# Kernel tuning notes

Measured on AMD Instinct MI355X. Metric: run time of the kernel, lower is better.

## Reference

```python
import jax, jax.numpy as jnp
import numpy as np

NUM_BINS = 128  # 32 mid-band bins + 96 bottom-band bins
LN_EPS = 1e-5


def _mlp_scores(desc, W1, b1, g1, be1, W2, b2, Ws, bs):
    # Linear -> LayerNorm -> SiLU -> Linear -> score head
    h = desc @ W1 + b1
    mu = h.mean(-1, keepdims=True)
    var = h.var(-1, keepdims=True)
    h = (h - mu) * jax.lax.rsqrt(var + LN_EPS) * g1 + be1
    h = h * jax.nn.sigmoid(h)  # SiLU
    feat = h @ W2 + b2
    scores = (feat @ Ws + bs)[..., 0]  # [B, N]
    return scores


def _grid_ids(kpts, H, W):
    x = kpts[..., 0]
    y = kpts[..., 1]
    mid = (y > 0.2 * H) & (y <= 0.5 * H)
    btm = y > 0.5 * H
    mgx = jnp.clip((x / W * 8).astype(jnp.int32), 0, 7)
    mgy = jnp.clip(((y - 0.2 * H) / (0.3 * H) * 4).astype(jnp.int32), 0, 3)
    bgx = jnp.clip((x / W * 16).astype(jnp.int32), 0, 15)
    bgy = jnp.clip(((y - 0.5 * H) / (0.5 * H) * 6).astype(jnp.int32), 0, 5)
    gid = jnp.where(btm, 32 + bgy * 16 + bgx, jnp.where(mid, mgy * 8 + mgx, -1))
    return gid  # [B, N], -1 = not in any grid band


def _select_one(scores, gid, top_k):
    # strict-'>' loop in the original), then compact + top-k fallback.
    N = scores.shape[0]
    valid = gid >= 0
    seg = jnp.where(valid, gid, NUM_BINS)  # dump invalid pts in dummy bin
    binmax = jax.ops.segment_max(scores, seg, num_segments=NUM_BINS + 1)
    is_win = valid & (scores == binmax[seg])
    winner_idx = jax.ops.segment_min(
        jnp.where(is_win, jnp.arange(N), N), seg, num_segments=NUM_BINS + 1
    )[:NUM_BINS]  # N = empty bin sentinel
    bin_valid = winner_idx < N
    # stable sort: non-empty bins first, preserving bin order
    order = jnp.argsort((~bin_valid).astype(jnp.int32))
    winners = winner_idx[order]  # [NUM_BINS], trailing sentinels
    num_sel = jnp.sum(bin_valid)
    # mask out already-selected winners, top-k fallback on the rest
    win_mask = jnp.zeros(N, bool).at[jnp.where(bin_valid, winner_idx, N)].set(True, mode='drop')
    rem = jnp.where(win_mask, -1e10, scores)
    _, extra = jax.lax.top_k(rem, top_k)
    j = jnp.arange(top_k)
    sel = jnp.where(
        j < num_sel,
        winners[jnp.clip(j, 0, NUM_BINS - 1)],
        extra[jnp.clip(j - num_sel, 0, top_k - 1)],
    )
    return sel  # [top_k]


def setup_inputs() -> dict:
    key = jax.random.key(0)
    ks = jax.random.split(key, 4)
    B, N, IN, OUT = 8, 50000, 256, 128
    H, W = 376, 1241
    kpts = jax.random.uniform(ks[0], (B, N, 2), jnp.float32) * jnp.array([W, H], jnp.float32)
    desc = jax.random.normal(ks[1], (B, N, IN), jnp.float32)
    kw = jax.random.split(ks[2], 3)
    W1 = 0.01 * jax.random.normal(kw[0], (IN, 256), jnp.float32)
    b1 = jnp.zeros((256,), jnp.float32)
    g1 = jnp.ones((256,), jnp.float32)
    be1 = jnp.zeros((256,), jnp.float32)
    W2 = 0.01 * jax.random.normal(kw[1], (256, OUT), jnp.float32)
    b2 = jnp.zeros((OUT,), jnp.float32)
    Ws = 0.001 * jax.random.normal(kw[2], (OUT, 1), jnp.float32)
    bs = jnp.zeros((1,), jnp.float32)
    return {"kpts": kpts, "desc": desc, "H": H, "W": W, "top_k": 128,
            "W1": W1, "b1": b1, "g1": g1, "be1": be1,
            "W2": W2, "b2": b2, "Ws": Ws, "bs": bs}


def reference(kpts, desc, H, W, top_k, W1, b1, g1, be1, W2, b2, Ws, bs):
    scores = _mlp_scores(desc, W1, b1, g1, be1, W2, b2, Ws, bs)  # [B,N]
    gid = _grid_ids(kpts, H, W)  # [B,N]
    indices = jax.vmap(lambda s, g: _select_one(s, g, top_k))(scores, gid)  # [B,top_k]
    final_feat = jnp.take_along_axis(desc, indices[:, :, None], axis=1)  # [B,top_k,256]
    final_kpts = jnp.take_along_axis(kpts, indices[:, :, None], axis=1)  # [B,top_k,2]
    return final_feat, final_kpts, indices
```

## Files before the change

kernel.cpp:

```cpp
#include <hip/hip_runtime.h>
#include <hip/hip_bf16.h>

typedef short bf16x8 __attribute__((ext_vector_type(8)));
typedef float f32x16 __attribute__((ext_vector_type(16)));

__device__ __forceinline__ unsigned short f2bf(float x) {
    unsigned u = __float_as_uint(x);
    return (unsigned short)((u + 0x7FFFu + ((u >> 16) & 1u)) >> 16);
}
__device__ __forceinline__ float bf2f(unsigned short h) {
    return __uint_as_float(((unsigned)h) << 16);
}
__device__ __forceinline__ unsigned score_key(float s) {
    unsigned u = __float_as_uint(s);
    return (u & 0x80000000u) ? ~u : (u | 0x80000000u);
}

__device__ __forceinline__ void split8n(const float4& fa, const float4& fb,
                                        bf16x8& hv, bf16x8& lv) {
    const float f[8] = {fa.x, fa.y, fa.z, fa.w, fb.x, fb.y, fb.z, fb.w};
    union { unsigned short u[8]; bf16x8 v; } H, L;
#pragma unroll
    for (int j = 0; j < 8; ++j) {
        __hip_bfloat16 hb = __float2bfloat16(f[j]);
        const unsigned short hr = reinterpret_cast<const unsigned short&>(hb);
        const float hf = __uint_as_float(((unsigned)hr) << 16);
        __hip_bfloat16 lb = __float2bfloat16(f[j] - hf);
        H.u[j] = hr;
        L.u[j] = reinterpret_cast<const unsigned short&>(lb);
    }
    hv = H.v; lv = L.v;
}

__device__ __forceinline__ void async_cp16(const uint4* g, uint4* l) {
    __builtin_amdgcn_global_load_lds(
        (const __attribute__((address_space(1))) unsigned int*)g,
        (__attribute__((address_space(3))) unsigned int*)l, 16, 0, 0);
}

__global__ void prep_kernel(const float* __restrict__ W2, const float* __restrict__ b2,
                            const float* __restrict__ Ws, const float* __restrict__ bs,
                            float* __restrict__ v, int OUT) {
    int j = threadIdx.x;
    float acc = 0.f;
    for (int o = 0; o < OUT; ++o) acc += W2[j * OUT + o] * Ws[o];
    v[j] = acc;
    if (j == 0) {
        float c = bs[0];
        for (int o = 0; o < OUT; ++o) c += b2[o] * Ws[o];
        v[256] = c;
    }
}

__global__ void prep_w1frag(const float* __restrict__ W1, uint4* __restrict__ wfrag) {
    const int s = blockIdx.x * 256 + threadIdx.x;
    const int kt = s >> 11;
    const int c = (s >> 6) & 31;
    const int lane = s & 63;
    const int hl = c >> 4;
    const int nt = (c >> 1) & 7;
    const int kc = c & 1;
    const int col = nt * 32 + (lane & 31);
    const int k0 = kt * 32 + kc * 16 + (lane >> 5) * 8;
    unsigned pk[4];
#pragma unroll
    for (int q = 0; q < 4; ++q) {
        float x0 = W1[(size_t)(k0 + 2 * q) * 256 + col];
        float x1 = W1[(size_t)(k0 + 2 * q + 1) * 256 + col];
        unsigned short a0, a1;
        if (hl == 0) { a0 = f2bf(x0); a1 = f2bf(x1); }
        else {
            a0 = f2bf(x0 - bf2f(f2bf(x0)));
            a1 = f2bf(x1 - bf2f(f2bf(x1)));
        }
        pk[q] = (unsigned)a0 | ((unsigned)a1 << 16);
    }
    wfrag[s] = make_uint4(pk[0], pk[1], pk[2], pk[3]);
}

__global__ void init_bins(unsigned long long* __restrict__ bins, int n) {
    int i = blockIdx.x * blockDim.x + threadIdx.x;
    if (i < n) bins[i] = 0ULL;
}

__global__ __launch_bounds__(512, 4) void score_kernel(
    const float* __restrict__ desc, const float* __restrict__ kpts,
    const uint4* __restrict__ wfrag,
    const float* __restrict__ b1, const float* __restrict__ g1, const float* __restrict__ be1,
    const int* __restrict__ Hp, const int* __restrict__ Wp,
    const float* __restrict__ v,
    float* __restrict__ scores, unsigned long long* __restrict__ bins,
    int N, int total)
{
    __shared__ uint4 BS[2][32 * 64];
    __shared__ float b1L[256], g1L[256], beL[256], vL[256];
    __shared__ float sums2[128][4];
    __shared__ float dot2[128][2];

    const int t = threadIdx.x;
    const int lane = t & 63;
    const int w = t >> 6;
    const int rg = w >> 1, cg = w & 1;
    const int c31 = lane & 31;
    const int h = lane >> 5;
    const int R0 = blockIdx.x * 128 + rg * 32;
    const int C0 = cg * 128;

    if (t < 256) { b1L[t] = b1[t]; g1L[t] = g1[t]; beL[t] = be1[t]; vL[t] = v[t]; }

    {
        const uint4* bsrc = wfrag + t;
#pragma unroll
        for (int j = 0; j < 4; ++j)
            async_cp16(bsrc + j * 512, &BS[0][j * 512 + t]);
    }

    const int rA = min(R0 + c31, total - 1);
    const float* pa = desc + (size_t)rA * 256 + h * 8;
    float4 a0A = *(const float4*)(pa + 0);
    float4 a0B = *(const float4*)(pa + 4);

    __syncthreads();

    f32x16 acc[4];
#pragma unroll
    for (int n4 = 0; n4 < 4; ++n4) {
        const float bc = b1L[C0 + n4 * 32 + c31];
#pragma unroll
        for (int r = 0; r < 16; ++r) acc[n4][r] = bc;
    }

    for (int kt = 0; kt < 8; ++kt) {
        const int cur = kt & 1;
        const float* pc = pa + kt * 32 + 16;
        float4 a1A = *(const float4*)(pc + 0);
        float4 a1B = *(const float4*)(pc + 4);
        float4 n0A, n0B;
        if (kt < 7) {
            const float* pn = pa + (kt + 1) * 32;
            n0A = *(const float4*)(pn + 0);
            n0B = *(const float4*)(pn + 4);
        }
        if (kt < 7) {
            const uint4* bsrc = wfrag + (size_t)(kt + 1) * 2048 + t;
#pragma unroll
            for (int j = 0; j < 4; ++j)
                async_cp16(bsrc + j * 512, &BS[cur ^ 1][j * 512 + t]);
        }
        {
            bf16x8 ah, al;
            split8n(a0A, a0B, ah, al);
            bf16x8 bh[4], bl[4];
#pragma unroll
            for (int n4 = 0; n4 < 4; ++n4) {
                const int nt = cg * 4 + n4;
                bh[n4] = *(const bf16x8*)&BS[cur][(nt * 2 + 0) * 64 + lane];
                bl[n4] = *(const bf16x8*)&BS[cur][(16 + nt * 2 + 0) * 64 + lane];
            }
#pragma unroll
            for (int n4 = 0; n4 < 4; ++n4)
                acc[n4] = __builtin_amdgcn_mfma_f32_32x32x16_bf16(ah, bh[n4], acc[n4], 0, 0, 0);
#pragma unroll
            for (int n4 = 0; n4 < 4; ++n4)
                acc[n4] = __builtin_amdgcn_mfma_f32_32x32x16_bf16(al, bh[n4], acc[n4], 0, 0, 0);
#pragma unroll
            for (int n4 = 0; n4 < 4; ++n4)
                acc[n4] = __builtin_amdgcn_mfma_f32_32x32x16_bf16(ah, bl[n4], acc[n4], 0, 0, 0);
#pragma unroll
            for (int n4 = 0; n4 < 4; ++n4)
                acc[n4] = __builtin_amdgcn_mfma_f32_32x32x16_bf16(al, bl[n4], acc[n4], 0, 0, 0);
        }
        {
            bf16x8 ah, al;
            split8n(a1A, a1B, ah, al);
            bf16x8 bh[4], bl[4];
#pragma unroll
            for (int n4 = 0; n4 < 4; ++n4) {
                const int nt = cg * 4 + n4;
                bh[n4] = *(const bf16x8*)&BS[cur][(nt * 2 + 1) * 64 + lane];
                bl[n4] = *(const bf16x8*)&BS[cur][(16 + nt * 2 + 1) * 64 + lane];
            }
#pragma unroll
            for (int n4 = 0; n4 < 4; ++n4)
                acc[n4] = __builtin_amdgcn_mfma_f32_32x32x16_bf16(ah, bh[n4], acc[n4], 0, 0, 0);
#pragma unroll
            for (int n4 = 0; n4 < 4; ++n4)
                acc[n4] = __builtin_amdgcn_mfma_f32_32x32x16_bf16(al, bh[n4], acc[n4], 0, 0, 0);
#pragma unroll
            for (int n4 = 0; n4 < 4; ++n4)
                acc[n4] = __builtin_amdgcn_mfma_f32_32x32x16_bf16(ah, bl[n4], acc[n4], 0, 0, 0);
#pragma unroll
            for (int n4 = 0; n4 < 4; ++n4)
                acc[n4] = __builtin_amdgcn_mfma_f32_32x32x16_bf16(al, bl[n4], acc[n4], 0, 0, 0);
        }
        a0A = n0A; a0B = n0B;
        __syncthreads();
    }

    float gE[4], beE[4], vE[4];
#pragma unroll
    for (int n4 = 0; n4 < 4; ++n4) {
        const int c = C0 + n4 * 32 + c31;
        gE[n4] = g1L[c]; beE[n4] = beL[c]; vE[n4] = vL[c];
    }
#pragma unroll
    for (int reg = 0; reg < 16; ++reg) {
        float sx = 0.f, sq = 0.f;
#pragma unroll
        for (int n4 = 0; n4 < 4; ++n4) {
            const float x = acc[n4][reg];
            sx += x; sq = fmaf(x, x, sq);
        }
#pragma unroll
        for (int m = 1; m <= 16; m <<= 1) {
            sx += __shfl_xor(sx, m);
            sq += __shfl_xor(sq, m);
        }
        if (c31 == 0) {
            const int rowB = rg * 32 + (reg & 3) + 8 * (reg >> 2) + 4 * h;
            sums2[rowB][cg * 2 + 0] = sx;
            sums2[rowB][cg * 2 + 1] = sq;
        }
    }
    __syncthreads();
#pragma unroll
    for (int reg = 0; reg < 16; ++reg) {
        const int rowB = rg * 32 + (reg & 3) + 8 * (reg >> 2) + 4 * h;
        const float4 s4 = *(const float4*)&sums2[rowB][0];
        const float mu = (s4.x + s4.z) * (1.f / 256.f);
        const float var = (s4.y + s4.w) * (1.f / 256.f) - mu * mu;
        const float rs = 1.f / sqrtf(var + 1e-5f);
        float dot = 0.f;
#pragma unroll
        for (int n4 = 0; n4 < 4; ++n4) {
            const float hv = (acc[n4][reg] - mu) * rs * gE[n4] + beE[n4];
            const float sg = 1.f / (1.f + __expf(-hv));
            dot = fmaf(vE[n4], hv * sg, dot);
        }
#pragma unroll
        for (int m = 1; m <= 16; m <<= 1) dot += __shfl_xor(dot, m);
        if (c31 == 0) dot2[rowB][cg] = dot;
    }
    __syncthreads();
    if (t < 128) {
        const int row = blockIdx.x * 128 + t;
        if (row < total) {
            const float sc = dot2[t][0] + dot2[t][1] + v[256];
            scores[row] = sc;
            const float Wf = (float)Wp[0];
            const int Hi = Hp[0];
            const float t02 = (float)(0.2 * (double)Hi);
            const float t05 = (float)(0.5 * (double)Hi);
            const float t03 = (float)(0.3 * (double)Hi);
            const float x = kpts[(size_t)row * 2 + 0];
            const float y = kpts[(size_t)row * 2 + 1];
            int g = -1;
            if (y > t05) {
                int bgx = (int)(x / Wf * 16.f); bgx = min(max(bgx, 0), 15);
                int bgy = (int)((y - t05) / t05 * 6.f); bgy = min(max(bgy, 0), 5);
                g = 32 + bgy * 16 + bgx;
            } else if (y > t02) {
                int mgx = (int)(x / Wf * 8.f); mgx = min(max(mgx, 0), 7);
                int mgy = (int)((y - t02) / t03 * 4.f); mgy = min(max(mgy, 0), 3);
                g = mgy * 8 + mgx;
            }
            if (g >= 0) {
                const int bb = row / N;
                const int n = row - bb * N;
                const unsigned long long pk =
                    ((unsigned long long)score_key(sc) << 32) | (unsigned)(~(unsigned)n);
                atomicMax(&bins[bb * 128 + g], pk);
            }
        }
    }
}

__global__ __launch_bounds__(256) void finalize_kernel(
    const float* __restrict__ scores, const unsigned long long* __restrict__ bins,
    const float* __restrict__ desc, const float* __restrict__ kpts,
    const int* __restrict__ tkp, float* __restrict__ out, int B, int N)
{
    const int b = blockIdx.x, t = threadIdx.x;
    const int topk = tkp[0];
    __shared__ int selL[512];
    __shared__ int nselS;
    __shared__ unsigned long long red[256];
    __shared__ unsigned long long binL[128];

    if (t < 128) binL[t] = bins[b * 128 + t];
    __syncthreads();
    if (t == 0) {
        int c = 0;
        for (int i = 0; i < 128; ++i)
            if ((binL[i] >> 32) != 0ULL) selL[c++] = (int)(~(unsigned)binL[i]);
        nselS = c;
    }
    __syncthreads();
    const int nsel = nselS;

    for (int need = nsel; need < topk; ++need) {
        unsigned long long best = 0ULL;
        for (int i = t; i < N; i += 256) {
            bool taken = false;
            for (int s2 = 0; s2 < need; ++s2)
                if (selL[s2] == i) { taken = true; break; }
            if (!taken) {
                const unsigned long long pk =
                    ((unsigned long long)score_key(scores[(size_t)b * N + i]) << 32)
                    | (unsigned)(~(unsigned)i);
                if (pk > best) best = pk;
            }
        }
        red[t] = best;
        __syncthreads();
        for (int off = 128; off > 0; off >>= 1) {
            if (t < off) { if (red[t + off] > red[t]) red[t] = red[t + off]; }
            __syncthreads();
        }
        if (t == 0) selL[need] = (int)(~(unsigned)red[0]);
        __syncthreads();
    }

    float* o_feat = out;
    float* o_kpts = out + (size_t)B * topk * 256;
    float* o_idx  = out + (size_t)B * topk * 258;
    for (int e = t; e < topk * 64; e += 256) {
        const int j = e >> 6, q4 = e & 63;
        const int n = selL[j];
        *(float4*)&o_feat[((size_t)b * topk + j) * 256 + q4 * 4] =
            *(const float4*)&desc[((size_t)b * N + n) * 256 + q4 * 4];
    }
    for (int j = t; j < topk; j += 256) {
        const int n = selL[j];
        o_kpts[((size_t)b * topk + j) * 2 + 0] = kpts[((size_t)b * N + n) * 2 + 0];
        o_kpts[((size_t)b * topk + j) * 2 + 1] = kpts[((size_t)b * N + n) * 2 + 1];
        o_idx[(size_t)b * topk + j] = (float)n;
    }
}

extern "C" void kernel_launch(void* const* d_in, const int* in_sizes, int n_in,
                              void* d_out, int out_size, void* d_ws, size_t ws_size,
                              hipStream_t stream) {
    const float* kpts = (const float*)d_in[0];
    const float* desc = (const float*)d_in[1];
    const int*   Hp   = (const int*)d_in[2];
    const int*   Wp   = (const int*)d_in[3];
    const int*   tkp  = (const int*)d_in[4];
    const float* W1   = (const float*)d_in[5];
    const float* b1   = (const float*)d_in[6];
    const float* g1   = (const float*)d_in[7];
    const float* be1  = (const float*)d_in[8];
    const float* W2   = (const float*)d_in[9];
    const float* b2   = (const float*)d_in[10];
    const float* Ws   = (const float*)d_in[11];
    const float* bs   = (const float*)d_in[12];

    const int total = in_sizes[1] / 256;
    const int BT    = out_size / 259;
    const int B     = BT / 128;
    const int N     = total / B;
    const int OUT   = in_sizes[11];

    float* ws_v      = (float*)d_ws;
    float* ws_scores = ws_v + 512;
    size_t off = ((size_t)(512 + total) * 4 + 255) & ~(size_t)255;
    unsigned long long* ws_bins = (unsigned long long*)((char*)d_ws + off);
    size_t off2 = (off + (size_t)B * 128 * 8 + 255) & ~(size_t)255;
    uint4* ws_wfrag = (uint4*)((char*)d_ws + off2);

    prep_kernel<<<1, 256, 0, stream>>>(W2, b2, Ws, bs, ws_v, OUT);
    prep_w1frag<<<64, 256, 0, stream>>>(W1, ws_wfrag);
    init_bins<<<(B * 128 + 255) / 256, 256, 0, stream>>>(ws_bins, B * 128);
    score_kernel<<<(total + 127) / 128, 512, 0, stream>>>(
        desc, kpts, ws_wfrag, b1, g1, be1, Hp, Wp, ws_v, ws_scores, ws_bins, N, total);
    finalize_kernel<<<B, 256, 0, stream>>>(ws_scores, ws_bins, desc, kpts, tkp,
                                           (float*)d_out, B, N);
}
```

Measured before the change: 401.2 us.

## Stage desc tiles in swizzled LDS and double rows per block in score kernel

The score kernel now handles 256 rows per block instead of 128. Each warp computes two 32-row M tiles, so every W1 fragment loaded from LDS feeds twice as many MFMAs. Desc tiles are now staged into a double-buffered, XOR-swizzled LDS buffer with manual waitcnt pipelining, raised wave priority around the MFMA bursts, and a hand-written bf16 split. Register and LDS use grow substantially and launch bounds drop to 2 blocks per CU, so occupancy and latency hiding may suffer.

```diff
diff --git a/kernel.cpp b/kernel.cpp
--- a/kernel.cpp
+++ b/kernel.cpp
@@ -1,5 +1,4 @@
 #include <hip/hip_runtime.h>
-#include <hip/hip_bf16.h>
 
 typedef short bf16x8 __attribute__((ext_vector_type(8)));
 typedef float f32x16 __attribute__((ext_vector_type(16)));
@@ -15,23 +14,21 @@
     unsigned u = __float_as_uint(s);
     return (u & 0x80000000u) ? ~u : (u | 0x80000000u);
 }
-
-__device__ __forceinline__ void split8n(const float4& fa, const float4& fb,
+__device__ __forceinline__ void split8m(const float4& fa, const float4& fb,
                                         bf16x8& hv, bf16x8& lv) {
     const float f[8] = {fa.x, fa.y, fa.z, fa.w, fb.x, fb.y, fb.z, fb.w};
-    union { unsigned short u[8]; bf16x8 v; } H, L;
-#pragma unroll
-    for (int j = 0; j < 8; ++j) {
-        __hip_bfloat16 hb = __float2bfloat16(f[j]);
-        const unsigned short hr = reinterpret_cast<const unsigned short&>(hb);
-        const float hf = __uint_as_float(((unsigned)hr) << 16);
-        __hip_bfloat16 lb = __float2bfloat16(f[j] - hf);
-        H.u[j] = hr;
-        L.u[j] = reinterpret_cast<const unsigned short&>(lb);
+    union { unsigned w[4]; bf16x8 v; } H, L;
+#pragma unroll
+    for (int q = 0; q < 4; ++q) {
+        const float x0 = f[2 * q], x1 = f[2 * q + 1];
+        const unsigned short h0 = f2bf(x0), h1 = f2bf(x1);
+        const unsigned short l0 = f2bf(x0 - bf2f(h0));
+        const unsigned short l1 = f2bf(x1 - bf2f(h1));
+        H.w[q] = (unsigned)h0 | ((unsigned)h1 << 16);
+        L.w[q] = (unsigned)l0 | ((unsigned)l1 << 16);
     }
     hv = H.v; lv = L.v;
 }
-
 __device__ __forceinline__ void async_cp16(const uint4* g, uint4* l) {
     __builtin_amdgcn_global_load_lds(
         (const __attribute__((address_space(1))) unsigned int*)g,
@@ -83,7 +80,7 @@
     if (i < n) bins[i] = 0ULL;
 }
 
-__global__ __launch_bounds__(512, 4) void score_kernel(
+__global__ __launch_bounds__(512, 2) void score_kernel(
     const float* __restrict__ desc, const float* __restrict__ kpts,
     const uint4* __restrict__ wfrag,
     const float* __restrict__ b1, const float* __restrict__ g1, const float* __restrict__ be1,
@@ -92,10 +89,10 @@
     float* __restrict__ scores, unsigned long long* __restrict__ bins,
     int N, int total)
 {
-    __shared__ uint4 BS[2][32 * 64];
-    __shared__ float b1L[256], g1L[256], beL[256], vL[256];
-    __shared__ float sums2[128][4];
-    __shared__ float dot2[128][2];
+    __shared__ uint4 BS[2][2048];
+    __shared__ float AS[2][256 * 32];
+    __shared__ float sums2[256][4];
+    __shared__ float dot2[256][2];
 
     const int t = threadIdx.x;
     const int lane = t & 63;
@@ -103,147 +100,167 @@
     const int rg = w >> 1, cg = w & 1;
     const int c31 = lane & 31;
     const int h = lane >> 5;
-    const int R0 = blockIdx.x * 128 + rg * 32;
-    const int C0 = cg * 128;
-
-    if (t < 256) { b1L[t] = b1[t]; g1L[t] = g1[t]; beL[t] = be1[t]; vL[t] = v[t]; }
-
+    const int R0T = blockIdx.x * 256;
+
+    int arow[4], alds[4];
+    const float* asrc[4];
+#pragma unroll
+    for (int j = 0; j < 4; ++j) {
+        const int u = j * 512 + t;
+        const int r = u >> 3, ck = u & 7;
+        arow[j] = r;
+        alds[j] = r * 32 + ((ck ^ (r & 7)) << 2);
+        asrc[j] = desc + (size_t)min(R0T + r, total - 1) * 256 + ck * 4;
+    }
+
+    f32x16 acc[2][4];
+#pragma unroll
+    for (int m = 0; m < 2; ++m)
+#pragma unroll
+        for (int j = 0; j < 4; ++j) {
+            const float bc = b1[cg * 128 + j * 32 + c31];
+#pragma unroll
+            for (int r = 0; r < 16; ++r) acc[m][j][r] = bc;
+        }
+
+    uint4 Acur[4], Anxt[4];
     {
-        const uint4* bsrc = wfrag + t;
-#pragma unroll
-        for (int j = 0; j < 4; ++j)
-            async_cp16(bsrc + j * 512, &BS[0][j * 512 + t]);
-    }
-
-    const int rA = min(R0 + c31, total - 1);
-    const float* pa = desc + (size_t)rA * 256 + h * 8;
-    float4 a0A = *(const float4*)(pa + 0);
-    float4 a0B = *(const float4*)(pa + 4);
-
-    __syncthreads();
-
-    f32x16 acc[4];
-#pragma unroll
-    for (int n4 = 0; n4 < 4; ++n4) {
-        const float bc = b1L[C0 + n4 * 32 + c31];
-#pragma unroll
-        for (int r = 0; r < 16; ++r) acc[n4][r] = bc;
-    }
-
+#pragma unroll
+        for (int js = 0; js < 4; ++js)
+            async_cp16(wfrag + js * 512 + t, &BS[0][js * 512 + t]);
+#pragma unroll
+        for (int j = 0; j < 4; ++j) Acur[j] = *(const uint4*)(asrc[j]);
+        asm volatile("s_waitcnt vmcnt(0)" ::: "memory");
+#pragma unroll
+        for (int j = 0; j < 4; ++j) *(uint4*)&AS[0][alds[j]] = Acur[j];
+#pragma unroll
+        for (int j = 0; j < 4; ++j) Acur[j] = *(const uint4*)(asrc[j] + 32);
+        asm volatile("s_waitcnt lgkmcnt(0)" ::: "memory");
+        __builtin_amdgcn_sched_barrier(0);
+        __builtin_amdgcn_s_barrier();
+    }
+
+    const int rowL0 = rg * 64 + c31;
+    const int swz = c31 & 7;
+
+#pragma unroll
     for (int kt = 0; kt < 8; ++kt) {
         const int cur = kt & 1;
-        const float* pc = pa + kt * 32 + 16;
-        float4 a1A = *(const float4*)(pc + 0);
-        float4 a1B = *(const float4*)(pc + 4);
-        float4 n0A, n0B;
+#pragma unroll
+        for (int kc = 0; kc < 2; ++kc) {
+            bf16x8 ah[2], al[2];
+#pragma unroll
+            for (int m = 0; m < 2; ++m) {
+                const int row = rowL0 + m * 32;
+                const int base = kc * 4 + h * 2;
+                const float4 f0 = *(const float4*)&AS[cur][row * 32 + ((base ^ swz) << 2)];
+                const float4 f1 = *(const float4*)&AS[cur][row * 32 + (((base + 1) ^ swz) << 2)];
+                split8m(f0, f1, ah[m], al[m]);
+            }
+            bf16x8 bh[4], bl[4];
+#pragma unroll
+            for (int j = 0; j < 4; ++j) {
+                const int ch = (cg * 4 + j) * 2 + kc;
+                bh[j] = *(const bf16x8*)&BS[cur][ch * 64 + lane];
+                bl[j] = *(const bf16x8*)&BS[cur][(16 + ch) * 64 + lane];
+            }
+            if (kt < 7) {
+#pragma unroll
+                for (int js = 0; js < 2; ++js) {
+                    const int slot = kc * 2 + js;
+                    async_cp16(wfrag + (size_t)(kt + 1) * 2048 + slot * 512 + t,
+                               &BS[cur ^ 1][slot * 512 + t]);
+                }
+            }
+            if (kc == 1 && kt < 6) {
+#pragma unroll
+                for (int j = 0; j < 4; ++j)
+                    Anxt[j] = *(const uint4*)(asrc[j] + (kt + 2) * 32);
+            }
+            __builtin_amdgcn_s_barrier();
+            __builtin_amdgcn_s_setprio(1);
+#pragma unroll
+            for (int p = 0; p < 4; ++p)
+#pragma unroll
+                for (int m = 0; m < 2; ++m)
+#pragma unroll
+                    for (int j = 0; j < 4; ++j) {
+                        const bf16x8 pa = (p & 2) ? al[m] : ah[m];
+                        const bf16x8 pb = (p & 1) ? bl[j] : bh[j];
+                        acc[m][j] = __builtin_amdgcn_mfma_f32_32x32x16_bf16(pa, pb, acc[m][j], 0, 0, 0);
+                    }
+            __builtin_amdgcn_s_setprio(0);
+            __builtin_amdgcn_s_barrier();
+        }
         if (kt < 7) {
-            const float* pn = pa + (kt + 1) * 32;
-            n0A = *(const float4*)(pn + 0);
-            n0B = *(const float4*)(pn + 4);
-        }
-        if (kt < 7) {
-            const uint4* bsrc = wfrag + (size_t)(kt + 1) * 2048 + t;
-#pragma unroll
-            for (int j = 0; j < 4; ++j)
-                async_cp16(bsrc + j * 512, &BS[cur ^ 1][j * 512 + t]);
-        }
-        {
-            bf16x8 ah, al;
-            split8n(a0A, a0B, ah, al);
-            bf16x8 bh[4], bl[4];
-#pragma unroll
-            for (int n4 = 0; n4 < 4; ++n4) {
-                const int nt = cg * 4 + n4;
-                bh[n4] = *(const bf16x8*)&BS[cur][(nt * 2 + 0) * 64 + lane];
-                bl[n4] = *(const bf16x8*)&BS[cur][(16 + nt * 2 + 0) * 64 + lane];
-            }
-#pragma unroll
-            for (int n4 = 0; n4 < 4; ++n4)
-                acc[n4] = __builtin_amdgcn_mfma_f32_32x32x16_bf16(ah, bh[n4], acc[n4], 0, 0, 0);
-#pragma unroll
-            for (int n4 = 0; n4 < 4; ++n4)
-                acc[n4] = __builtin_amdgcn_mfma_f32_32x32x16_bf16(al, bh[n4], acc[n4], 0, 0, 0);
-#pragma unroll
-            for (int n4 = 0; n4 < 4; ++n4)
-                acc[n4] = __builtin_amdgcn_mfma_f32_32x32x16_bf16(ah, bl[n4], acc[n4], 0, 0, 0);
-#pragma unroll
-            for (int n4 = 0; n4 < 4; ++n4)
-                acc[n4] = __builtin_amdgcn_mfma_f32_32x32x16_bf16(al, bl[n4], acc[n4], 0, 0, 0);
-        }
-        {
-            bf16x8 ah, al;
-            split8n(a1A, a1B, ah, al);
-            bf16x8 bh[4], bl[4];
-#pragma unroll
-            for (int n4 = 0; n4 < 4; ++n4) {
-                const int nt = cg * 4 + n4;
-                bh[n4] = *(const bf16x8*)&BS[cur][(nt * 2 + 1) * 64 + lane];
-                bl[n4] = *(const bf16x8*)&BS[cur][(16 + nt * 2 + 1) * 64 + lane];
-            }
-#pragma unroll
-            for (int n4 = 0; n4 < 4; ++n4)
-                acc[n4] = __builtin_amdgcn_mfma_f32_32x32x16_bf16(ah, bh[n4], acc[n4], 0, 0, 0);
-#pragma unroll
-            for (int n4 = 0; n4 < 4; ++n4)
-                acc[n4] = __builtin_amdgcn_mfma_f32_32x32x16_bf16(al, bh[n4], acc[n4], 0, 0, 0);
-#pragma unroll
-            for (int n4 = 0; n4 < 4; ++n4)
-                acc[n4] = __builtin_amdgcn_mfma_f32_32x32x16_bf16(ah, bl[n4], acc[n4], 0, 0, 0);
-#pragma unroll
-            for (int n4 = 0; n4 < 4; ++n4)
-                acc[n4] = __builtin_amdgcn_mfma_f32_32x32x16_bf16(al, bl[n4], acc[n4], 0, 0, 0);
-        }
-        a0A = n0A; a0B = n0B;
-        __syncthreads();
+            if (kt < 6) asm volatile("s_waitcnt vmcnt(8)" ::: "memory");
+            else        asm volatile("s_waitcnt vmcnt(4)" ::: "memory");
+#pragma unroll
+            for (int j = 0; j < 4; ++j) *(uint4*)&AS[cur ^ 1][alds[j]] = Acur[j];
+            if (kt < 6) {
+#pragma unroll
+                for (int j = 0; j < 4; ++j) Acur[j] = Anxt[j];
+            }
+            asm volatile("s_waitcnt lgkmcnt(0)" ::: "memory");
+            __builtin_amdgcn_sched_barrier(0);
+            if (kt < 6) asm volatile("s_waitcnt vmcnt(4)" ::: "memory");
+            else        asm volatile("s_waitcnt vmcnt(0)" ::: "memory");
+            __builtin_amdgcn_s_barrier();
+        }
     }
 
     float gE[4], beE[4], vE[4];
 #pragma unroll
-    for (int n4 = 0; n4 < 4; ++n4) {
-        const int c = C0 + n4 * 32 + c31;
-        gE[n4] = g1L[c]; beE[n4] = beL[c]; vE[n4] = vL[c];
-    }
-#pragma unroll
-    for (int reg = 0; reg < 16; ++reg) {
-        float sx = 0.f, sq = 0.f;
-#pragma unroll
-        for (int n4 = 0; n4 < 4; ++n4) {
-            const float x = acc[n4][reg];
-            sx += x; sq = fmaf(x, x, sq);
-        }
-#pragma unroll
-        for (int m = 1; m <= 16; m <<= 1) {
-            sx += __shfl_xor(sx, m);
-            sq += __shfl_xor(sq, m);
-        }
-        if (c31 == 0) {
-            const int rowB = rg * 32 + (reg & 3) + 8 * (reg >> 2) + 4 * h;
-            sums2[rowB][cg * 2 + 0] = sx;
-            sums2[rowB][cg * 2 + 1] = sq;
-        }
-    }
-    __syncthreads();
-#pragma unroll
-    for (int reg = 0; reg < 16; ++reg) {
-        const int rowB = rg * 32 + (reg & 3) + 8 * (reg >> 2) + 4 * h;
-        const float4 s4 = *(const float4*)&sums2[rowB][0];
-        const float mu = (s4.x + s4.z) * (1.f / 256.f);
-        const float var = (s4.y + s4.w) * (1.f / 256.f) - mu * mu;
-        const float rs = 1.f / sqrtf(var + 1e-5f);
-        float dot = 0.f;
-#pragma unroll
-        for (int n4 = 0; n4 < 4; ++n4) {
-            const float hv = (acc[n4][reg] - mu) * rs * gE[n4] + beE[n4];
-            const float sg = 1.f / (1.f + __expf(-hv));
-            dot = fmaf(vE[n4], hv * sg, dot);
-        }
-#pragma unroll
-        for (int m = 1; m <= 16; m <<= 1) dot += __shfl_xor(dot, m);
-        if (c31 == 0) dot2[rowB][cg] = dot;
-    }
-    __syncthreads();
-    if (t < 128) {
-        const int row = blockIdx.x * 128 + t;
+    for (int j = 0; j < 4; ++j) {
+        const int c = cg * 128 + j * 32 + c31;
+        gE[j] = g1[c]; beE[j] = be1[c]; vE[j] = v[c];
+    }
+    __syncthreads();
+#pragma unroll
+    for (int m = 0; m < 2; ++m)
+#pragma unroll
+        for (int reg = 0; reg < 16; ++reg) {
+            float sx = 0.f, sq = 0.f;
+#pragma unroll
+            for (int j = 0; j < 4; ++j) {
+                const float x = acc[m][j][reg];
+                sx += x; sq = fmaf(x, x, sq);
+            }
+#pragma unroll
+            for (int msk = 1; msk <= 16; msk <<= 1) {
+                sx += __shfl_xor(sx, msk);
+                sq += __shfl_xor(sq, msk);
+            }
+            if (c31 == 0) {
+                const int rowB = rg * 64 + m * 32 + (reg & 3) + 8 * (reg >> 2) + 4 * h;
+                sums2[rowB][cg * 2 + 0] = sx;
+                sums2[rowB][cg * 2 + 1] = sq;
+            }
+        }
+    __syncthreads();
+#pragma unroll
+    for (int m = 0; m < 2; ++m)
+#pragma unroll
+        for (int reg = 0; reg < 16; ++reg) {
+            const int rowB = rg * 64 + m * 32 + (reg & 3) + 8 * (reg >> 2) + 4 * h;
+            const float4 s4 = *(const float4*)&sums2[rowB][0];
+            const float mu = (s4.x + s4.z) * (1.f / 256.f);
+            const float var = (s4.y + s4.w) * (1.f / 256.f) - mu * mu;
+            const float rs = 1.f / sqrtf(var + 1e-5f);
+            float dot = 0.f;
+#pragma unroll
+            for (int j = 0; j < 4; ++j) {
+                const float hv = (acc[m][j][reg] - mu) * rs * gE[j] + beE[j];
+                const float sg = 1.f / (1.f + __expf(-hv));
+                dot = fmaf(vE[j], hv * sg, dot);
+            }
+#pragma unroll
+            for (int msk = 1; msk <= 16; msk <<= 1) dot += __shfl_xor(dot, msk);
+            if (c31 == 0) dot2[rowB][cg] = dot;
+        }
+    __syncthreads();
+    if (t < 256) {
+        const int row = R0T + t;
         if (row < total) {
             const float sc = dot2[t][0] + dot2[t][1] + v[256];
             scores[row] = sc;
@@ -371,7 +388,7 @@
     prep_kernel<<<1, 256, 0, stream>>>(W2, b2, Ws, bs, ws_v, OUT);
     prep_w1frag<<<64, 256, 0, stream>>>(W1, ws_wfrag);
     init_bins<<<(B * 128 + 255) / 256, 256, 0, stream>>>(ws_bins, B * 128);
-    score_kernel<<<(total + 127) / 128, 512, 0, stream>>>(
+    score_kernel<<<(total + 255) / 256, 512, 0, stream>>>(
         desc, kpts, ws_wfrag, b1, g1, be1, Hp, Wp, ws_v, ws_scores, ws_bins, N, total);
     finalize_kernel<<<B, 256, 0, stream>>>(ws_scores, ws_bins, desc, kpts, tkp,
                                            (float*)d_out, B, N);
```

Result: slower. 531.7 us (+32.5%).

## Score with single bf16 MFMA pass and refine near-max bin candidates in fp32

Applied to the files above, without the earlier changes.

Replaces the hi/lo split-bf16 GEMM, which issued four MFMAs per tile, with a single truncated-bf16 pass. This cuts MFMA work and halves the W1 fragment traffic. A new refine kernel recomputes the full fp32 MLP score, but only for points whose approximate score lies within a heuristic margin (sum|v|/128) of their bin maximum, and re-selects the bin winners from those exact scores. The risk is that the margin is not a rigorous error bound, and the top-k fallback still ranks by the approximate scores, so selections may differ from the reference.

```diff
diff --git a/kernel.cpp b/kernel.cpp
--- a/kernel.cpp
+++ b/kernel.cpp
@@ -1,5 +1,4 @@
 #include <hip/hip_runtime.h>
-#include <hip/hip_bf16.h>
 
 typedef short bf16x8 __attribute__((ext_vector_type(8)));
 typedef float f32x16 __attribute__((ext_vector_type(16)));
@@ -8,30 +7,24 @@
     unsigned u = __float_as_uint(x);
     return (unsigned short)((u + 0x7FFFu + ((u >> 16) & 1u)) >> 16);
 }
-__device__ __forceinline__ float bf2f(unsigned short h) {
-    return __uint_as_float(((unsigned)h) << 16);
-}
 __device__ __forceinline__ unsigned score_key(float s) {
     unsigned u = __float_as_uint(s);
     return (u & 0x80000000u) ? ~u : (u | 0x80000000u);
 }
-
-__device__ __forceinline__ void split8n(const float4& fa, const float4& fb,
-                                        bf16x8& hv, bf16x8& lv) {
-    const float f[8] = {fa.x, fa.y, fa.z, fa.w, fb.x, fb.y, fb.z, fb.w};
-    union { unsigned short u[8]; bf16x8 v; } H, L;
-#pragma unroll
-    for (int j = 0; j < 8; ++j) {
-        __hip_bfloat16 hb = __float2bfloat16(f[j]);
-        const unsigned short hr = reinterpret_cast<const unsigned short&>(hb);
-        const float hf = __uint_as_float(((unsigned)hr) << 16);
-        __hip_bfloat16 lb = __float2bfloat16(f[j] - hf);
-        H.u[j] = hr;
-        L.u[j] = reinterpret_cast<const unsigned short&>(lb);
-    }
-    hv = H.v; lv = L.v;
-}
-
+__device__ __forceinline__ float key2float(unsigned k) {
+    return (k & 0x80000000u) ? __uint_as_float(k ^ 0x80000000u) : __uint_as_float(~k);
+}
+__device__ __forceinline__ bf16x8 hi8(const float4& a, const float4& b) {
+    union { unsigned w[4]; bf16x8 v; } H;
+    const float f[8] = {a.x, a.y, a.z, a.w, b.x, b.y, b.z, b.w};
+#pragma unroll
+    for (int q = 0; q < 4; ++q) {
+        const unsigned u0 = __float_as_uint(f[2 * q]);
+        const unsigned u1 = __float_as_uint(f[2 * q + 1]);
+        H.w[q] = (u0 >> 16) | (u1 & 0xFFFF0000u);
+    }
+    return H.v;
+}
 __device__ __forceinline__ void async_cp16(const uint4* g, uint4* l) {
     __builtin_amdgcn_global_load_lds(
         (const __attribute__((address_space(1))) unsigned int*)g,
@@ -41,41 +34,39 @@
 __global__ void prep_kernel(const float* __restrict__ W2, const float* __restrict__ b2,
                             const float* __restrict__ Ws, const float* __restrict__ bs,
                             float* __restrict__ v, int OUT) {
+    __shared__ float vL[256];
     int j = threadIdx.x;
     float acc = 0.f;
     for (int o = 0; o < OUT; ++o) acc += W2[j * OUT + o] * Ws[o];
     v[j] = acc;
+    vL[j] = fabsf(acc);
+    __syncthreads();
     if (j == 0) {
         float c = bs[0];
         for (int o = 0; o < OUT; ++o) c += b2[o] * Ws[o];
         v[256] = c;
-    }
-}
-
-__global__ void prep_w1frag(const float* __restrict__ W1, uint4* __restrict__ wfrag) {
+        float sa = 0.f;
+        for (int o = 0; o < 256; ++o) sa += vL[o];
+        v[257] = fmaxf(1e-5f, sa * (1.f / 128.f));
+    }
+}
+
+__global__ void prep_w1fragH(const float* __restrict__ W1, uint4* __restrict__ wf) {
     const int s = blockIdx.x * 256 + threadIdx.x;
-    const int kt = s >> 11;
-    const int c = (s >> 6) & 31;
+    const int kt = s >> 10;
+    const int c = (s >> 6) & 15;
     const int lane = s & 63;
-    const int hl = c >> 4;
-    const int nt = (c >> 1) & 7;
-    const int kc = c & 1;
+    const int nt = c >> 1, kc = c & 1;
     const int col = nt * 32 + (lane & 31);
     const int k0 = kt * 32 + kc * 16 + (lane >> 5) * 8;
     unsigned pk[4];
 #pragma unroll
     for (int q = 0; q < 4; ++q) {
-        float x0 = W1[(size_t)(k0 + 2 * q) * 256 + col];
-        float x1 = W1[(size_t)(k0 + 2 * q + 1) * 256 + col];
-        unsigned short a0, a1;
-        if (hl == 0) { a0 = f2bf(x0); a1 = f2bf(x1); }
-        else {
-            a0 = f2bf(x0 - bf2f(f2bf(x0)));
-            a1 = f2bf(x1 - bf2f(f2bf(x1)));
-        }
-        pk[q] = (unsigned)a0 | ((unsigned)a1 << 16);
-    }
-    wfrag[s] = make_uint4(pk[0], pk[1], pk[2], pk[3]);
+        const float x0 = W1[(size_t)(k0 + 2 * q) * 256 + col];
+        const float x1 = W1[(size_t)(k0 + 2 * q + 1) * 256 + col];
+        pk[q] = (unsigned)f2bf(x0) | ((unsigned)f2bf(x1) << 16);
+    }
+    wf[s] = make_uint4(pk[0], pk[1], pk[2], pk[3]);
 }
 
 __global__ void init_bins(unsigned long long* __restrict__ bins, int n) {
@@ -85,14 +76,14 @@
 
 __global__ __launch_bounds__(512, 4) void score_kernel(
     const float* __restrict__ desc, const float* __restrict__ kpts,
-    const uint4* __restrict__ wfrag,
+    const uint4* __restrict__ wfragH,
     const float* __restrict__ b1, const float* __restrict__ g1, const float* __restrict__ be1,
     const int* __restrict__ Hp, const int* __restrict__ Wp,
     const float* __restrict__ v,
-    float* __restrict__ scores, unsigned long long* __restrict__ bins,
-    int N, int total)
+    float* __restrict__ scores, unsigned char* __restrict__ gid8,
+    unsigned long long* __restrict__ bins, int N, int total)
 {
-    __shared__ uint4 BS[2][32 * 64];
+    __shared__ uint4 BS[2][1024];
     __shared__ float b1L[256], g1L[256], beL[256], vL[256];
     __shared__ float sums2[128][4];
     __shared__ float dot2[128][2];
@@ -108,12 +99,8 @@
 
     if (t < 256) { b1L[t] = b1[t]; g1L[t] = g1[t]; beL[t] = be1[t]; vL[t] = v[t]; }
 
-    {
-        const uint4* bsrc = wfrag + t;
-#pragma unroll
-        for (int j = 0; j < 4; ++j)
-            async_cp16(bsrc + j * 512, &BS[0][j * 512 + t]);
-    }
+    async_cp16(wfragH + t, &BS[0][t]);
+    async_cp16(wfragH + 512 + t, &BS[0][512 + t]);
 
     const int rA = min(R0 + c31, total - 1);
     const float* pa = desc + (size_t)rA * 256 + h * 8;
@@ -140,58 +127,28 @@
             const float* pn = pa + (kt + 1) * 32;
             n0A = *(const float4*)(pn + 0);
             n0B = *(const float4*)(pn + 4);
-        }
-        if (kt < 7) {
-            const uint4* bsrc = wfrag + (size_t)(kt + 1) * 2048 + t;
+            async_cp16(wfragH + (size_t)(kt + 1) * 1024 + t, &BS[cur ^ 1][t]);
+            async_cp16(wfragH + (size_t)(kt + 1) * 1024 + 512 + t, &BS[cur ^ 1][512 + t]);
+        }
+        {
+            const bf16x8 ah = hi8(a0A, a0B);
+            bf16x8 bh[4];
 #pragma unroll
             for (int j = 0; j < 4; ++j)
-                async_cp16(bsrc + j * 512, &BS[cur ^ 1][j * 512 + t]);
+                bh[j] = *(const bf16x8*)&BS[cur][((cg * 4 + j) * 2 + 0) * 64 + lane];
+#pragma unroll
+            for (int j = 0; j < 4; ++j)
+                acc[j] = __builtin_amdgcn_mfma_f32_32x32x16_bf16(ah, bh[j], acc[j], 0, 0, 0);
         }
         {
-            bf16x8 ah, al;
-            split8n(a0A, a0B, ah, al);
-            bf16x8 bh[4], bl[4];
-#pragma unroll
-            for (int n4 = 0; n4 < 4; ++n4) {
-                const int nt = cg * 4 + n4;
-                bh[n4] = *(const bf16x8*)&BS[cur][(nt * 2 + 0) * 64 + lane];
-                bl[n4] = *(const bf16x8*)&BS[cur][(16 + nt * 2 + 0) * 64 + lane];
-            }
-#pragma unroll
-            for (int n4 = 0; n4 < 4; ++n4)
-                acc[n4] = __builtin_amdgcn_mfma_f32_32x32x16_bf16(ah, bh[n4], acc[n4], 0, 0, 0);
-#pragma unroll
-            for (int n4 = 0; n4 < 4; ++n4)
-                acc[n4] = __builtin_amdgcn_mfma_f32_32x32x16_bf16(al, bh[n4], acc[n4], 0, 0, 0);
-#pragma unroll
-            for (int n4 = 0; n4 < 4; ++n4)
-                acc[n4] = __builtin_amdgcn_mfma_f32_32x32x16_bf16(ah, bl[n4], acc[n4], 0, 0, 0);
-#pragma unroll
-            for (int n4 = 0; n4 < 4; ++n4)
-                acc[n4] = __builtin_amdgcn_mfma_f32_32x32x16_bf16(al, bl[n4], acc[n4], 0, 0, 0);
-        }
-        {
-            bf16x8 ah, al;
-            split8n(a1A, a1B, ah, al);
-            bf16x8 bh[4], bl[4];
-#pragma unroll
-            for (int n4 = 0; n4 < 4; ++n4) {
-                const int nt = cg * 4 + n4;
-                bh[n4] = *(const bf16x8*)&BS[cur][(nt * 2 + 1) * 64 + lane];
-                bl[n4] = *(const bf16x8*)&BS[cur][(16 + nt * 2 + 1) * 64 + lane];
-            }
-#pragma unroll
-            for (int n4 = 0; n4 < 4; ++n4)
-                acc[n4] = __builtin_amdgcn_mfma_f32_32x32x16_bf16(ah, bh[n4], acc[n4], 0, 0, 0);
-#pragma unroll
-            for (int n4 = 0; n4 < 4; ++n4)
-                acc[n4] = __builtin_amdgcn_mfma_f32_32x32x16_bf16(al, bh[n4], acc[n4], 0, 0, 0);
-#pragma unroll
-            for (int n4 = 0; n4 < 4; ++n4)
-                acc[n4] = __builtin_amdgcn_mfma_f32_32x32x16_bf16(ah, bl[n4], acc[n4], 0, 0, 0);
-#pragma unroll
-            for (int n4 = 0; n4 < 4; ++n4)
-                acc[n4] = __builtin_amdgcn_mfma_f32_32x32x16_bf16(al, bl[n4], acc[n4], 0, 0, 0);
+            const bf16x8 ah = hi8(a1A, a1B);
+            bf16x8 bh[4];
+#pragma unroll
+            for (int j = 0; j < 4; ++j)
+                bh[j] = *(const bf16x8*)&BS[cur][((cg * 4 + j) * 2 + 1) * 64 + lane];
+#pragma unroll
+            for (int j = 0; j < 4; ++j)
+                acc[j] = __builtin_amdgcn_mfma_f32_32x32x16_bf16(ah, bh[j], acc[j], 0, 0, 0);
         }
         a0A = n0A; a0B = n0B;
         __syncthreads();
@@ -264,6 +221,7 @@
                 int mgy = (int)((y - t02) / t03 * 4.f); mgy = min(max(mgy, 0), 3);
                 g = mgy * 8 + mgx;
             }
+            gid8[row] = (unsigned char)(g < 0 ? 255 : g);
             if (g >= 0) {
                 const int bb = row / N;
                 const int n = row - bb * N;
@@ -275,8 +233,84 @@
     }
 }
 
+__global__ __launch_bounds__(256, 4) void refine_kernel(
+    const float* __restrict__ desc, const float* __restrict__ scores,
+    const unsigned char* __restrict__ gid8, const unsigned long long* __restrict__ bins,
+    unsigned long long* __restrict__ exbins,
+    const float* __restrict__ W1, const float* __restrict__ b1,
+    const float* __restrict__ g1, const float* __restrict__ be1,
+    const float* __restrict__ v, int N, int total)
+{
+    __shared__ int list[128];
+    __shared__ int cnt;
+    __shared__ float dL[256];
+    __shared__ float red[16];
+
+    const int t = threadIdx.x;
+    const int lane = t & 63;
+    const int w = t >> 6;
+    const int R0 = blockIdx.x * 128;
+    if (t == 0) cnt = 0;
+    __syncthreads();
+    const float Delta = v[257];
+
+    if (t < 128) {
+        const int row = R0 + t;
+        if (row < total) {
+            const unsigned char gv = gid8[row];
+            if (gv != 255) {
+                const int bb = row / N;
+                const unsigned mk = (unsigned)(bins[bb * 128 + gv] >> 32);
+                if (scores[row] >= key2float(mk) - Delta) {
+                    const int p = atomicAdd(&cnt, 1);
+                    list[p] = row;
+                }
+            }
+        }
+    }
+    __syncthreads();
+    const int nq = cnt;
+
+    for (int c = 0; c < nq; ++c) {
+        const int row = list[c];
+        dL[t] = desc[(size_t)row * 256 + t];
+        __syncthreads();
+        float hj = b1[t];
+        const float* wp = W1 + t;
+#pragma unroll 8
+        for (int k = 0; k < 256; ++k) hj = fmaf(dL[k], wp[(size_t)k * 256], hj);
+        float sx = hj, sq = hj * hj;
+#pragma unroll
+        for (int m = 1; m <= 32; m <<= 1) {
+            sx += __shfl_xor(sx, m);
+            sq += __shfl_xor(sq, m);
+        }
+        if (lane == 0) { red[w] = sx; red[8 + w] = sq; }
+        __syncthreads();
+        const float mu = (red[0] + red[1] + red[2] + red[3]) * (1.f / 256.f);
+        const float var = (red[8] + red[9] + red[10] + red[11]) * (1.f / 256.f) - mu * mu;
+        const float rs = 1.f / sqrtf(var + 1e-5f);
+        const float y = (hj - mu) * rs * g1[t] + be1[t];
+        float p = v[t] * (y / (1.f + __expf(-y)));
+#pragma unroll
+        for (int m = 1; m <= 32; m <<= 1) p += __shfl_xor(p, m);
+        if (lane == 0) red[w] = p;
+        __syncthreads();
+        if (t == 0) {
+            const float se = red[0] + red[1] + red[2] + red[3] + v[256];
+            const int bb = row / N;
+            const int n = row - bb * N;
+            const int g = gid8[row];
+            const unsigned long long pk =
+                ((unsigned long long)score_key(se) << 32) | (unsigned)(~(unsigned)n);
+            atomicMax(&exbins[bb * 128 + g], pk);
+        }
+        __syncthreads();
+    }
+}
+
 __global__ __launch_bounds__(256) void finalize_kernel(
-    const float* __restrict__ scores, const unsigned long long* __restrict__ bins,
+    const float* __restrict__ scores, const unsigned long long* __restrict__ exbins,
     const float* __restrict__ desc, const float* __restrict__ kpts,
     const int* __restrict__ tkp, float* __restrict__ out, int B, int N)
 {
@@ -287,7 +321,7 @@
     __shared__ unsigned long long red[256];
     __shared__ unsigned long long binL[128];
 
-    if (t < 128) binL[t] = bins[b * 128 + t];
+    if (t < 128) binL[t] = exbins[b * 128 + t];
     __syncthreads();
     if (t == 0) {
         int c = 0;
@@ -363,16 +397,24 @@
 
     float* ws_v      = (float*)d_ws;
     float* ws_scores = ws_v + 512;
-    size_t off = ((size_t)(512 + total) * 4 + 255) & ~(size_t)255;
-    unsigned long long* ws_bins = (unsigned long long*)((char*)d_ws + off);
-    size_t off2 = (off + (size_t)B * 128 * 8 + 255) & ~(size_t)255;
-    uint4* ws_wfrag = (uint4*)((char*)d_ws + off2);
+    size_t offg = ((size_t)(512 + total) * 4 + 255) & ~(size_t)255;
+    unsigned char* ws_gid8 = (unsigned char*)d_ws + offg;
+    size_t offb = (offg + (size_t)total + 255) & ~(size_t)255;
+    unsigned long long* ws_bins = (unsigned long long*)((char*)d_ws + offb);
+    unsigned long long* ws_exbins = ws_bins + (size_t)B * 128;
+    size_t offw = (offb + (size_t)2 * B * 128 * 8 + 255) & ~(size_t)255;
+    uint4* ws_wfragH = (uint4*)((char*)d_ws + offw);
+
+    const int nblk = (total + 127) / 128;
 
     prep_kernel<<<1, 256, 0, stream>>>(W2, b2, Ws, bs, ws_v, OUT);
-    prep_w1frag<<<64, 256, 0, stream>>>(W1, ws_wfrag);
-    init_bins<<<(B * 128 + 255) / 256, 256, 0, stream>>>(ws_bins, B * 128);
-    score_kernel<<<(total + 127) / 128, 512, 0, stream>>>(
-        desc, kpts, ws_wfrag, b1, g1, be1, Hp, Wp, ws_v, ws_scores, ws_bins, N, total);
-    finalize_kernel<<<B, 256, 0, stream>>>(ws_scores, ws_bins, desc, kpts, tkp,
+    prep_w1fragH<<<32, 256, 0, stream>>>(W1, ws_wfragH);
+    init_bins<<<(2 * B * 128 + 255) / 256, 256, 0, stream>>>(ws_bins, 2 * B * 128);
+    score_kernel<<<nblk, 512, 0, stream>>>(
+        desc, kpts, ws_wfragH, b1, g1, be1, Hp, Wp, ws_v,
+        ws_scores, ws_gid8, ws_bins, N, total);
+    refine_kernel<<<nblk, 256, 0, stream>>>(
+        desc, ws_scores, ws_gid8, ws_bins, ws_exbins, W1, b1, g1, be1, ws_v, N, total);
+    finalize_kernel<<<B, 256, 0, stream>>>(ws_scores, ws_exbins, desc, kpts, tkp,
                                            (float*)d_out, B, N);
 }
```

After: 379.7 us. -5.4%, faster.
